# Kernel optimization log

Measured on AMD Instinct MI355X. Metric: run time of the kernel, lower is better.

Reference implementation:

```python
import jax, jax.numpy as jnp
import numpy as np

D = 1024      # input_dim == attention_dim == num_heads*head_dim
H = 16        # num_heads
HD = 64       # head_dim
FF = 4096     # ff_dim
EPS = 1e-5


def _layernorm(x, gamma, beta):
    mu = jnp.mean(x, axis=-1, keepdims=True)
    var = jnp.var(x, axis=-1, keepdims=True)
    return (x - mu) * jax.lax.rsqrt(var + EPS) * gamma + beta


def setup_inputs() -> dict:
    key = jax.random.key(0)
    ks = jax.random.split(key, 11)
    s_in = 1.0 / np.sqrt(D)
    s_ff = 1.0 / np.sqrt(FF)
    return {
        "x": jax.random.normal(ks[0], (2, 2048, D), dtype=jnp.float32),
        "w_qkv": jax.random.uniform(ks[1], (D, 3 * D), jnp.float32, -s_in, s_in),
        "b_qkv": jax.random.uniform(ks[2], (3 * D,), jnp.float32, -s_in, s_in),
        "w_o": jax.random.uniform(ks[3], (D, D), jnp.float32, -s_in, s_in),
        "b_o": jax.random.uniform(ks[4], (D,), jnp.float32, -s_in, s_in),
        "g1": jnp.ones((D,), jnp.float32),
        "be1": jnp.zeros((D,), jnp.float32),
        "w1": jax.random.uniform(ks[5], (D, FF), jnp.float32, -s_in, s_in),
        "b1": jax.random.uniform(ks[6], (FF,), jnp.float32, -s_in, s_in),
        "w2": jax.random.uniform(ks[7], (FF, D), jnp.float32, -s_ff, s_ff),
        "b2": jax.random.uniform(ks[8], (D,), jnp.float32, -s_ff, s_ff),
        "g2": jnp.ones((D,), jnp.float32),
        "be2": jnp.zeros((D,), jnp.float32),
    }


def reference(x, w_qkv, b_qkv, w_o, b_o, g1, be1, w1, b1, w2, b2, g2, be2):
    N, L, _ = x.shape
    qkv = x @ w_qkv + b_qkv                       # [N, L, 3D]
    q = qkv[..., :D].reshape(N, L, H, HD)
    k = qkv[..., D:2 * D].reshape(N, L, H, HD)
    v = qkv[..., 2 * D:].reshape(N, L, H, HD)
    scores = jnp.einsum('nqhd,nkhd->nhqk', q, k) / np.sqrt(HD)
    attn = jax.nn.softmax(scores, axis=-1)        # [N, H, L, L]
    out = jnp.einsum('nhql,nlhd->nqhd', attn, v).reshape(N, L, D)
    attn_out = out @ w_o + b_o
    # dropout is identity in eval mode
    h = _layernorm(attn_out + x, g1, be1)
    ff = jax.nn.relu(h @ w1 + b1) @ w2 + b2
    return _layernorm(h + ff, g2, be2)
```

## Files before the change

### kernel.cpp

```cpp
#include <hip/hip_runtime.h>
#include <cstddef>
#include <cstdint>

static constexpr int Dm   = 1024;
static constexpr int Hh   = 16;
static constexpr int HDd  = 64;
static constexpr int FFd  = 4096;
static constexpr int Ls   = 2048;
static constexpr int Nb   = 2;
static constexpr int Mrows = Nb * Ls;

typedef short bf16x8 __attribute__((ext_vector_type(8)));
typedef float f32x4  __attribute__((ext_vector_type(4)));

__device__ __forceinline__ ushort f2b(float f) {
    uint32_t u = __builtin_bit_cast(uint32_t, f);
    u = (u + 0x7FFFu + ((u >> 16) & 1u)) >> 16;
    return (ushort)u;
}
__device__ __forceinline__ ushort f2bf(float f) {
    return (ushort)((__builtin_bit_cast(uint32_t, f) + 0x8000u) >> 16);
}
__device__ __forceinline__ float b2f(ushort b) {
    return __builtin_bit_cast(float, (uint32_t)b << 16);
}

__device__ __forceinline__ void gl2lds16(const ushort* g, ushort* l) {
    __builtin_amdgcn_global_load_lds(
        (const __attribute__((address_space(1))) void*)g,
        (__attribute__((address_space(3))) void*)l, 16, 0, 0);
}

__global__ __launch_bounds__(256) void convert_bf16(
    const float* __restrict__ src, ushort* __restrict__ dst, int n)
{
    int i = (blockIdx.x * 256 + threadIdx.x) * 4;
    if (i >= n) return;
    float4 v = *(const float4*)(src + i);
    uint2 o;
    o.x = (uint32_t)f2b(v.x) | ((uint32_t)f2b(v.y) << 16);
    o.y = (uint32_t)f2b(v.z) | ((uint32_t)f2b(v.w) << 16);
    *(uint2*)(dst + i) = o;
}

__global__ __launch_bounds__(256) void transpose_bf16(
    const float* __restrict__ src, ushort* __restrict__ dst, int K, int N)
{
    __shared__ float t[32][33];
    const int k0 = blockIdx.y * 32, n0 = blockIdx.x * 32;
    const int tx = threadIdx.x & 31, ty = threadIdx.x >> 5;
    #pragma unroll
    for (int i = 0; i < 4; ++i)
        t[ty + i * 8][tx] = src[(size_t)(k0 + ty + i * 8) * N + n0 + tx];
    __syncthreads();
    #pragma unroll
    for (int i = 0; i < 4; ++i)
        dst[(size_t)(n0 + ty + i * 8) * K + k0 + tx] = f2b(t[tx][ty + i * 8]);
}

template <int TN, int RELU, int VOUT>
__global__ __launch_bounds__(256) void gemm_mfma(
    const ushort* __restrict__ A, const ushort* __restrict__ Bt,
    const float* __restrict__ bias,
    ushort* __restrict__ Cb, ushort* __restrict__ vT, int M, int N, int K)
{
    constexpr int NT  = TN / 32;
    constexpr int BSZ = TN * 32;
    __shared__ __align__(16) ushort As[2 * 128 * 32];
    __shared__ __align__(16) ushort Bs[2 * BSZ];

    const int tid  = threadIdx.x;
    const int bm   = blockIdx.y * 128, bn = blockIdx.x * TN;
    const int wave = tid >> 6, lane = tid & 63;
    const int wm = (wave & 1) * 64;
    const int wn = (wave >> 1) * (TN / 2);
    const int lr = lane & 15, lq = lane >> 4;

    const int rr = wave * 16 + (lane >> 2);
    const int sg = lane & 3;
    const ushort* Ag = A  + (size_t)(bm + rr) * K + sg * 8;
    const ushort* Bg = Bt + (size_t)(bn + rr) * K + sg * 8;

    f32x4 acc[4][NT];
    #pragma unroll
    for (int i = 0; i < 4; ++i)
        #pragma unroll
        for (int j = 0; j < NT; ++j)
            acc[i][j] = (f32x4){0.f, 0.f, 0.f, 0.f};

    gl2lds16(Ag,                  As + wave * 512);
    gl2lds16(Ag + (size_t)64 * K, As + 2048 + wave * 512);
    gl2lds16(Bg,                  Bs + wave * 512);
    if (TN == 128)
        gl2lds16(Bg + (size_t)64 * K, Bs + 2048 + wave * 512);

    int ib = 0;
    for (int k0 = 0; k0 < K; k0 += 32, ib ^= 1) {
        __syncthreads();
        if (k0 + 32 < K) {
            const int nb = ib ^ 1;
            gl2lds16(Ag + k0 + 32,                  As + nb * 4096 + wave * 512);
            gl2lds16(Ag + k0 + 32 + (size_t)64 * K, As + nb * 4096 + 2048 + wave * 512);
            gl2lds16(Bg + k0 + 32,                  Bs + nb * BSZ + wave * 512);
            if (TN == 128)
                gl2lds16(Bg + k0 + 32 + (size_t)64 * K, Bs + nb * BSZ + 2048 + wave * 512);
        }

        const ushort* Ar = As + ib * 4096;
        const ushort* Br = Bs + ib * BSZ;
        bf16x8 af[4], bf[NT];
        #pragma unroll
        for (int mt = 0; mt < 4; ++mt)
            af[mt] = *(const bf16x8*)(Ar + (wm + mt * 16 + lr) * 32 + lq * 8);
        #pragma unroll
        for (int nt = 0; nt < NT; ++nt)
            bf[nt] = *(const bf16x8*)(Br + (wn + nt * 16 + lr) * 32 + lq * 8);

        #pragma unroll
        for (int mt = 0; mt < 4; ++mt)
            #pragma unroll
            for (int nt = 0; nt < NT; ++nt)
                acc[mt][nt] = __builtin_amdgcn_mfma_f32_16x16x32_bf16(
                    af[mt], bf[nt], acc[mt][nt], 0, 0, 0);
    }

    if (VOUT && bn >= 2 * Dm) {
        #pragma unroll
        for (int nt = 0; nt < NT; ++nt) {
            const int n = bn + wn + nt * 16 + lr;
            const float bv = bias[n];
            const int col = n - 2 * Dm;
            const int h = col >> 6, d = col & 63;
            #pragma unroll
            for (int mt = 0; mt < 4; ++mt) {
                const int m0 = bm + wm + mt * 16 + lq * 4;
                const int batch = m0 >> 11, key0 = m0 & (Ls - 1);
                ushort4 ob;
                ushort* op = (ushort*)&ob;
                #pragma unroll
                for (int r = 0; r < 4; ++r) op[r] = f2bf(acc[mt][nt][r] + bv);
                *(ushort4*)(vT + (((size_t)(batch * Hh + h)) * HDd + d) * Ls + key0) = ob;
            }
        }
        return;
    }
    #pragma unroll
    for (int nt = 0; nt < NT; ++nt) {
        const int n = bn + wn + nt * 16 + lr;
        const float bv = bias[n];
        #pragma unroll
        for (int mt = 0; mt < 4; ++mt) {
            const int m0 = bm + wm + mt * 16 + lq * 4;
            #pragma unroll
            for (int r = 0; r < 4; ++r) {
                float v = acc[mt][nt][r] + bv;
                if (RELU) v = fmaxf(v, 0.0f);
                Cb[(size_t)(m0 + r) * N + n] = f2bf(v);
            }
        }
    }
}

__global__ __launch_bounds__(256) void attn_mfma(
    const ushort* __restrict__ qkv, const ushort* __restrict__ vT,
    ushort* __restrict__ out)
{
    const int tid = threadIdx.x, wave = tid >> 6, lane = tid & 63;
    const int lr = lane & 15, lq = lane >> 4;
    const int h = blockIdx.y, n = blockIdx.z;
    const int q0 = blockIdx.x * 128 + wave * 32;
    const size_t RS = 3 * Dm;
    const ushort* base  = qkv + (size_t)n * Ls * RS;
    const ushort* vbase = vT + (size_t)(n * Hh + h) * HDd * Ls;

    __shared__ __align__(16) ushort Kb[64 * 72];
    __shared__ __align__(16) ushort Vt[64 * 72];
    __shared__ __align__(16) ushort Pq[4][32 * 72];

    bf16x8 qf[2][2];
    {
        const float c = 0.18033688011112042f;
        #pragma unroll
        for (int qh = 0; qh < 2; ++qh) {
            const ushort* qg = base + (size_t)(q0 + qh * 16 + lr) * RS + h * HDd + lq * 8;
            bf16x8 t0 = *(const bf16x8*)(qg);
            bf16x8 t1 = *(const bf16x8*)(qg + 32);
            #pragma unroll
            for (int j = 0; j < 8; ++j) {
                qf[0][qh][j] = (short)f2b(b2f((ushort)t0[j]) * c);
                qf[1][qh][j] = (short)f2b(b2f((ushort)t1[j]) * c);
            }
        }
    }

    bf16x8 onesf;
    #pragma unroll
    for (int j = 0; j < 8; ++j) onesf[j] = (short)0x3F80;
    const f32x4 z4 = (f32x4){0.f, 0.f, 0.f, 0.f};

    f32x4 o[4][2];
    #pragma unroll
    for (int dt = 0; dt < 4; ++dt)
        #pragma unroll
        for (int qh = 0; qh < 2; ++qh)
            o[dt][qh] = (f32x4){0.f, 0.f, 0.f, 0.f};
    f32x4 dacc[2];
    dacc[0] = (f32x4){0.f, 0.f, 0.f, 0.f};
    dacc[1] = (f32x4){0.f, 0.f, 0.f, 0.f};

    const int srow = tid >> 2, ssg = tid & 3;
    const ushort* kg = base + (size_t)srow * RS + Dm + h * HDd;
    const ushort* vg = vbase + (size_t)srow * Ls;
    ushort* Pw = Pq[wave];

    int4 ka = *(const int4*)(kg + ssg * 8);
    int4 kb = *(const int4*)(kg + (ssg + 4) * 8);
    int4 va = *(const int4*)(vg + ssg * 8);
    int4 vb = *(const int4*)(vg + (ssg + 4) * 8);

    for (int kt = 0; kt < Ls; kt += 64) {
        __syncthreads();
        *(int4*)(Kb + srow * 72 + ssg * 8)       = ka;
        *(int4*)(Kb + srow * 72 + (ssg + 4) * 8) = kb;
        *(int4*)(Vt + srow * 72 + ssg * 8)       = va;
        *(int4*)(Vt + srow * 72 + (ssg + 4) * 8) = vb;
        __syncthreads();

        if (kt + 64 < Ls) {
            const ushort* kp = kg + (size_t)(kt + 64) * RS;
            const ushort* vp = vg + (kt + 64);
            ka = *(const int4*)(kp + ssg * 8);
            kb = *(const int4*)(kp + (ssg + 4) * 8);
            va = *(const int4*)(vp + ssg * 8);
            vb = *(const int4*)(vp + (ssg + 4) * 8);
        }

        f32x4 s[4][2];
        #pragma unroll
        for (int ks = 0; ks < 2; ++ks)
            #pragma unroll
            for (int mt = 0; mt < 4; ++mt) {
                bf16x8 kf = *(const bf16x8*)(Kb + (mt * 16 + lr) * 72 + ks * 32 + lq * 8);
                #pragma unroll
                for (int qh = 0; qh < 2; ++qh)
                    s[mt][qh] = __builtin_amdgcn_mfma_f32_16x16x32_bf16(
                        kf, qf[ks][qh], ks == 0 ? z4 : s[mt][qh], 0, 0, 0);
            }

        uint2 pb[4][2];
        #pragma unroll
        for (int mt = 0; mt < 4; ++mt)
            #pragma unroll
            for (int qh = 0; qh < 2; ++qh) {
                float p0 = exp2f(s[mt][qh][0]);
                float p1 = exp2f(s[mt][qh][1]);
                float p2 = exp2f(s[mt][qh][2]);
                float p3 = exp2f(s[mt][qh][3]);
                uint32_t w0, w1;
                asm("v_cvt_pk_bf16_f32 %0, %1, %2" : "=v"(w0) : "v"(p0), "v"(p1));
                asm("v_cvt_pk_bf16_f32 %0, %1, %2" : "=v"(w1) : "v"(p2), "v"(p3));
                pb[mt][qh].x = w0;
                pb[mt][qh].y = w1;
            }

        #pragma unroll
        for (int qh = 0; qh < 2; ++qh)
            #pragma unroll
            for (int mt = 0; mt < 4; ++mt)
                *(uint2*)(Pw + (qh * 16 + lr) * 72 + mt * 16 + lq * 4) = pb[mt][qh];

        #pragma unroll
        for (int ks = 0; ks < 2; ++ks) {
            bf16x8 pf[2];
            #pragma unroll
            for (int qh = 0; qh < 2; ++qh)
                pf[qh] = *(const bf16x8*)(Pw + (qh * 16 + lr) * 72 + ks * 32 + lq * 8);
            #pragma unroll
            for (int dt = 0; dt < 4; ++dt) {
                bf16x8 vf = *(const bf16x8*)(Vt + (dt * 16 + lr) * 72 + ks * 32 + lq * 8);
                #pragma unroll
                for (int qh = 0; qh < 2; ++qh)
                    o[dt][qh] = __builtin_amdgcn_mfma_f32_16x16x32_bf16(
                        vf, pf[qh], o[dt][qh], 0, 0, 0);
            }
            #pragma unroll
            for (int qh = 0; qh < 2; ++qh)
                dacc[qh] = __builtin_amdgcn_mfma_f32_16x16x32_bf16(
                    onesf, pf[qh], dacc[qh], 0, 0, 0);
        }
    }

    #pragma unroll
    for (int qh = 0; qh < 2; ++qh) {
        const float inv = 1.0f / dacc[qh][0];
        ushort* orow = out + (size_t)(n * Ls + q0 + qh * 16 + lr) * Dm + h * HDd;
        #pragma unroll
        for (int dt = 0; dt < 4; ++dt) {
            ushort4 ob;
            ushort* op = (ushort*)&ob;
            #pragma unroll
            for (int r = 0; r < 4; ++r) op[r] = f2bf(o[dt][qh][r] * inv);
            *(ushort4*)(orow + dt * 16 + lq * 4) = ob;
        }
    }
}

template <int A_BF16, int B_BF16, int OUT_F32>
__global__ __launch_bounds__(256) void add_ln(
    const void* __restrict__ a, const void* __restrict__ b,
    const float* __restrict__ gamma, const float* __restrict__ beta,
    float* __restrict__ outf, ushort* __restrict__ outb)
{
    const int row = blockIdx.x;
    const int tid = threadIdx.x;

    float va[4], vb[4];
    if (A_BF16) {
        ushort4 u = ((const ushort4*)((const ushort*)a + (size_t)row * Dm))[tid];
        va[0] = b2f(u.x); va[1] = b2f(u.y); va[2] = b2f(u.z); va[3] = b2f(u.w);
    } else {
        float4 f = ((const float4*)((const float*)a + (size_t)row * Dm))[tid];
        va[0] = f.x; va[1] = f.y; va[2] = f.z; va[3] = f.w;
    }
    if (B_BF16) {
        ushort4 u = ((const ushort4*)((const ushort*)b + (size_t)row * Dm))[tid];
        vb[0] = b2f(u.x); vb[1] = b2f(u.y); vb[2] = b2f(u.z); vb[3] = b2f(u.w);
    } else {
        float4 f = ((const float4*)((const float*)b + (size_t)row * Dm))[tid];
        vb[0] = f.x; vb[1] = f.y; vb[2] = f.z; vb[3] = f.w;
    }
    float v[4] = {va[0] + vb[0], va[1] + vb[1], va[2] + vb[2], va[3] + vb[3]};

    float s  = v[0] + v[1] + v[2] + v[3];
    float sq = v[0]*v[0] + v[1]*v[1] + v[2]*v[2] + v[3]*v[3];

    __shared__ float red[8];
    #pragma unroll
    for (int off = 32; off > 0; off >>= 1) {
        s  += __shfl_down(s, off);
        sq += __shfl_down(sq, off);
    }
    const int wv = tid >> 6;
    if ((tid & 63) == 0) { red[wv] = s; red[4 + wv] = sq; }
    __syncthreads();
    s  = red[0] + red[1] + red[2] + red[3];
    sq = red[4] + red[5] + red[6] + red[7];

    const float mu  = s * (1.0f / Dm);
    const float var = sq * (1.0f / Dm) - mu * mu;
    const float inv = rsqrtf(var + 1e-5f);

    const float4 g  = ((const float4*)gamma)[tid];
    const float4 be = ((const float4*)beta)[tid];
    float ov[4];
    ov[0] = (v[0] - mu) * inv * g.x + be.x;
    ov[1] = (v[1] - mu) * inv * g.y + be.y;
    ov[2] = (v[2] - mu) * inv * g.z + be.z;
    ov[3] = (v[3] - mu) * inv * g.w + be.w;
    if (OUT_F32) {
        float4 o4 = {ov[0], ov[1], ov[2], ov[3]};
        ((float4*)(outf + (size_t)row * Dm))[tid] = o4;
    } else {
        uint2 ob;
        ob.x = (uint32_t)f2bf(ov[0]) | ((uint32_t)f2bf(ov[1]) << 16);
        ob.y = (uint32_t)f2bf(ov[2]) | ((uint32_t)f2bf(ov[3]) << 16);
        *(uint2*)(outb + (size_t)row * Dm + tid * 4) = ob;
    }
}

extern "C" void kernel_launch(void* const* d_in, const int* in_sizes, int n_in,
                              void* d_out, int out_size, void* d_ws, size_t ws_size,
                              hipStream_t stream)
{
    const float* x     = (const float*)d_in[0];
    const float* w_qkv = (const float*)d_in[1];
    const float* b_qkv = (const float*)d_in[2];
    const float* w_o   = (const float*)d_in[3];
    const float* b_o   = (const float*)d_in[4];
    const float* g1    = (const float*)d_in[5];
    const float* be1   = (const float*)d_in[6];
    const float* w1    = (const float*)d_in[7];
    const float* b1    = (const float*)d_in[8];
    const float* w2    = (const float*)d_in[9];
    const float* b2    = (const float*)d_in[10];
    const float* g2    = (const float*)d_in[11];
    const float* be2   = (const float*)d_in[12];
    float* out = (float*)d_out;

    char* p = (char*)d_ws;
    ushort* qkvb  = (ushort*)p;  p += (size_t)Mrows * 3 * Dm * 2;
    ushort* attnb = (ushort*)p;  p += (size_t)Mrows * Dm * 2;
    ushort* projb = (ushort*)p;  p += (size_t)Mrows * Dm * 2;
    ushort* hb    = (ushort*)p;  p += (size_t)Mrows * Dm * 2;
    ushort* ffb   = (ushort*)p;  p += (size_t)Mrows * FFd * 2;
    ushort* ff2b  = (ushort*)p;  p += (size_t)Mrows * Dm * 2;
    ushort* xb    = (ushort*)p;  p += (size_t)Mrows * Dm * 2;
    ushort* wqkvT = (ushort*)p;  p += (size_t)(3 * Dm) * Dm * 2;
    ushort* woT   = (ushort*)p;  p += (size_t)Dm * Dm * 2;
    ushort* w1T   = (ushort*)p;  p += (size_t)FFd * Dm * 2;
    ushort* w2T   = (ushort*)p;  p += (size_t)Dm * FFd * 2;
    ushort* vTg   = (ushort*)p;  p += (size_t)Mrows * Dm * 2;

    convert_bf16<<<dim3(Mrows * Dm / 1024), dim3(256), 0, stream>>>(x, xb, Mrows * Dm);
    transpose_bf16<<<dim3(3 * Dm / 32, Dm / 32), dim3(256), 0, stream>>>(w_qkv, wqkvT, Dm, 3 * Dm);
    transpose_bf16<<<dim3(Dm / 32, Dm / 32),     dim3(256), 0, stream>>>(w_o, woT, Dm, Dm);
    transpose_bf16<<<dim3(FFd / 32, Dm / 32),    dim3(256), 0, stream>>>(w1, w1T, Dm, FFd);
    transpose_bf16<<<dim3(Dm / 32, FFd / 32),    dim3(256), 0, stream>>>(w2, w2T, FFd, Dm);

    gemm_mfma<128, 0, 1><<<dim3(3 * Dm / 128, Mrows / 128), dim3(256), 0, stream>>>(
        xb, wqkvT, b_qkv, qkvb, vTg, Mrows, 3 * Dm, Dm);

    attn_mfma<<<dim3(Ls / 128, Hh, Nb), dim3(256), 0, stream>>>(qkvb, vTg, attnb);

    gemm_mfma<64, 0, 0><<<dim3(Dm / 64, Mrows / 128), dim3(256), 0, stream>>>(
        attnb, woT, b_o, projb, nullptr, Mrows, Dm, Dm);

    add_ln<1, 0, 0><<<dim3(Mrows), dim3(256), 0, stream>>>(projb, x, g1, be1, nullptr, hb);

    gemm_mfma<128, 1, 0><<<dim3(FFd / 128, Mrows / 128), dim3(256), 0, stream>>>(
        hb, w1T, b1, ffb, nullptr, Mrows, FFd, Dm);

    gemm_mfma<64, 0, 0><<<dim3(Dm / 64, Mrows / 128), dim3(256), 0, stream>>>(
        ffb, w2T, b2, ff2b, nullptr, Mrows, Dm, FFd);

    add_ln<1, 1, 1><<<dim3(Mrows), dim3(256), 0, stream>>>(ff2b, hb, g2, be2, out, nullptr);
}
```

Before: 402.4 us.

## Split-K the N=1024 GEMMs, fold partial sums and bias into LayerNorm, swizzle blocks

```diff
diff --git a/kernel.cpp b/kernel.cpp
--- a/kernel.cpp
+++ b/kernel.cpp
@@ -58,7 +58,7 @@
         dst[(size_t)(n0 + ty + i * 8) * K + k0 + tx] = f2b(t[tx][ty + i * 8]);
 }
 
-template <int TN, int RELU, int VOUT>
+template <int TN, int RELU, int VOUT, int SPLITK>
 __global__ __launch_bounds__(256) void gemm_mfma(
     const ushort* __restrict__ A, const ushort* __restrict__ Bt,
     const float* __restrict__ bias,
@@ -70,16 +70,27 @@
     __shared__ __align__(16) ushort Bs[2 * BSZ];
 
     const int tid  = threadIdx.x;
-    const int bm   = blockIdx.y * 128, bn = blockIdx.x * TN;
+    int bx, by;
+    {
+        const int gx = gridDim.x;
+        const int nwg = gx * gridDim.y;
+        const int lin = blockIdx.y * gx + blockIdx.x;
+        const int swz = (lin & 7) * (nwg >> 3) + (lin >> 3);
+        by = swz / gx; bx = swz - by * gx;
+    }
+    const int bm   = by * 128, bn = bx * TN;
     const int wave = tid >> 6, lane = tid & 63;
     const int wm = (wave & 1) * 64;
     const int wn = (wave >> 1) * (TN / 2);
     const int lr = lane & 15, lq = lane >> 4;
 
+    const int KS   = K / SPLITK;
+    const int Koff = (SPLITK > 1) ? blockIdx.z * KS : 0;
+
     const int rr = wave * 16 + (lane >> 2);
     const int sg = lane & 3;
-    const ushort* Ag = A  + (size_t)(bm + rr) * K + sg * 8;
-    const ushort* Bg = Bt + (size_t)(bn + rr) * K + sg * 8;
+    const ushort* Ag = A  + (size_t)(bm + rr) * K + Koff + sg * 8;
+    const ushort* Bg = Bt + (size_t)(bn + rr) * K + Koff + sg * 8;
 
     f32x4 acc[4][NT];
     #pragma unroll
@@ -95,9 +106,9 @@
         gl2lds16(Bg + (size_t)64 * K, Bs + 2048 + wave * 512);
 
     int ib = 0;
-    for (int k0 = 0; k0 < K; k0 += 32, ib ^= 1) {
+    for (int k0 = 0; k0 < KS; k0 += 32, ib ^= 1) {
         __syncthreads();
-        if (k0 + 32 < K) {
+        if (k0 + 32 < KS) {
             const int nb = ib ^ 1;
             gl2lds16(Ag + k0 + 32,                  As + nb * 4096 + wave * 512);
             gl2lds16(Ag + k0 + 32 + (size_t)64 * K, As + nb * 4096 + 2048 + wave * 512);
@@ -124,6 +135,21 @@
                     af[mt], bf[nt], acc[mt][nt], 0, 0, 0);
     }
 
+    if (SPLITK > 1) {
+        ushort* Cp = Cb + (size_t)blockIdx.z * M * N;
+        #pragma unroll
+        for (int nt = 0; nt < NT; ++nt) {
+            const int n = bn + wn + nt * 16 + lr;
+            #pragma unroll
+            for (int mt = 0; mt < 4; ++mt) {
+                const int m0 = bm + wm + mt * 16 + lq * 4;
+                #pragma unroll
+                for (int r = 0; r < 4; ++r)
+                    Cp[(size_t)(m0 + r) * N + n] = f2bf(acc[mt][nt][r]);
+            }
+        }
+        return;
+    }
     if (VOUT && bn >= 2 * Dm) {
         #pragma unroll
         for (int nt = 0; nt < NT; ++nt) {
@@ -167,8 +193,13 @@
 {
     const int tid = threadIdx.x, wave = tid >> 6, lane = tid & 63;
     const int lr = lane & 15, lq = lane >> 4;
-    const int h = blockIdx.y, n = blockIdx.z;
-    const int q0 = blockIdx.x * 128 + wave * 32;
+    int bx, h, n;
+    {
+        const int lin = (blockIdx.z * 16 + blockIdx.y) * 16 + blockIdx.x;
+        const int swz = (lin & 7) * 64 + (lin >> 3);
+        bx = swz & 15; h = (swz >> 4) & 15; n = swz >> 8;
+    }
+    const int q0 = bx * 128 + wave * 32;
     const size_t RS = 3 * Dm;
     const ushort* base  = qkv + (size_t)n * Ls * RS;
     const ushort* vbase = vT + (size_t)(n * Hh + h) * HDd * Ls;
@@ -305,31 +336,33 @@
     }
 }
 
-template <int A_BF16, int B_BF16, int OUT_F32>
-__global__ __launch_bounds__(256) void add_ln(
-    const void* __restrict__ a, const void* __restrict__ b,
+template <int OTHER_BF16, int OUT_F32>
+__global__ __launch_bounds__(256) void add3_ln(
+    const ushort* __restrict__ part, const void* __restrict__ other,
+    const float* __restrict__ bias,
     const float* __restrict__ gamma, const float* __restrict__ beta,
     float* __restrict__ outf, ushort* __restrict__ outb)
 {
     const int row = blockIdx.x;
     const int tid = threadIdx.x;
 
-    float va[4], vb[4];
-    if (A_BF16) {
-        ushort4 u = ((const ushort4*)((const ushort*)a + (size_t)row * Dm))[tid];
-        va[0] = b2f(u.x); va[1] = b2f(u.y); va[2] = b2f(u.z); va[3] = b2f(u.w);
+    ushort4 u0 = ((const ushort4*)(part + (size_t)row * Dm))[tid];
+    ushort4 u1 = ((const ushort4*)(part + (size_t)Mrows * Dm + (size_t)row * Dm))[tid];
+    float4  bv = ((const float4*)bias)[tid];
+
+    float vo[4];
+    if (OTHER_BF16) {
+        ushort4 u = ((const ushort4*)((const ushort*)other + (size_t)row * Dm))[tid];
+        vo[0] = b2f(u.x); vo[1] = b2f(u.y); vo[2] = b2f(u.z); vo[3] = b2f(u.w);
     } else {
-        float4 f = ((const float4*)((const float*)a + (size_t)row * Dm))[tid];
-        va[0] = f.x; va[1] = f.y; va[2] = f.z; va[3] = f.w;
-    }
-    if (B_BF16) {
-        ushort4 u = ((const ushort4*)((const ushort*)b + (size_t)row * Dm))[tid];
-        vb[0] = b2f(u.x); vb[1] = b2f(u.y); vb[2] = b2f(u.z); vb[3] = b2f(u.w);
-    } else {
-        float4 f = ((const float4*)((const float*)b + (size_t)row * Dm))[tid];
-        vb[0] = f.x; vb[1] = f.y; vb[2] = f.z; vb[3] = f.w;
-    }
-    float v[4] = {va[0] + vb[0], va[1] + vb[1], va[2] + vb[2], va[3] + vb[3]};
+        float4 f = ((const float4*)((const float*)other + (size_t)row * Dm))[tid];
+        vo[0] = f.x; vo[1] = f.y; vo[2] = f.z; vo[3] = f.w;
+    }
+    float v[4];
+    v[0] = b2f(u0.x) + b2f(u1.x) + bv.x + vo[0];
+    v[1] = b2f(u0.y) + b2f(u1.y) + bv.y + vo[1];
+    v[2] = b2f(u0.z) + b2f(u1.z) + bv.z + vo[2];
+    v[3] = b2f(u0.w) + b2f(u1.w) + bv.w + vo[3];
 
     float s  = v[0] + v[1] + v[2] + v[3];
     float sq = v[0]*v[0] + v[1]*v[1] + v[2]*v[2] + v[3]*v[3];
@@ -390,10 +423,9 @@
     char* p = (char*)d_ws;
     ushort* qkvb  = (ushort*)p;  p += (size_t)Mrows * 3 * Dm * 2;
     ushort* attnb = (ushort*)p;  p += (size_t)Mrows * Dm * 2;
-    ushort* projb = (ushort*)p;  p += (size_t)Mrows * Dm * 2;
+    ushort* part  = (ushort*)p;  p += (size_t)2 * Mrows * Dm * 2;
     ushort* hb    = (ushort*)p;  p += (size_t)Mrows * Dm * 2;
     ushort* ffb   = (ushort*)p;  p += (size_t)Mrows * FFd * 2;
-    ushort* ff2b  = (ushort*)p;  p += (size_t)Mrows * Dm * 2;
     ushort* xb    = (ushort*)p;  p += (size_t)Mrows * Dm * 2;
     ushort* wqkvT = (ushort*)p;  p += (size_t)(3 * Dm) * Dm * 2;
     ushort* woT   = (ushort*)p;  p += (size_t)Dm * Dm * 2;
@@ -407,21 +439,23 @@
     transpose_bf16<<<dim3(FFd / 32, Dm / 32),    dim3(256), 0, stream>>>(w1, w1T, Dm, FFd);
     transpose_bf16<<<dim3(Dm / 32, FFd / 32),    dim3(256), 0, stream>>>(w2, w2T, FFd, Dm);
 
-    gemm_mfma<128, 0, 1><<<dim3(3 * Dm / 128, Mrows / 128), dim3(256), 0, stream>>>(
+    gemm_mfma<128, 0, 1, 1><<<dim3(3 * Dm / 128, Mrows / 128), dim3(256), 0, stream>>>(
         xb, wqkvT, b_qkv, qkvb, vTg, Mrows, 3 * Dm, Dm);
 
     attn_mfma<<<dim3(Ls / 128, Hh, Nb), dim3(256), 0, stream>>>(qkvb, vTg, attnb);
 
-    gemm_mfma<64, 0, 0><<<dim3(Dm / 64, Mrows / 128), dim3(256), 0, stream>>>(
-        attnb, woT, b_o, projb, nullptr, Mrows, Dm, Dm);
-
-    add_ln<1, 0, 0><<<dim3(Mrows), dim3(256), 0, stream>>>(projb, x, g1, be1, nullptr, hb);
-
-    gemm_mfma<128, 1, 0><<<dim3(FFd / 128, Mrows / 128), dim3(256), 0, stream>>>(
+    gemm_mfma<64, 0, 0, 2><<<dim3(Dm / 64, Mrows / 128, 2), dim3(256), 0, stream>>>(
+        attnb, woT, nullptr, part, nullptr, Mrows, Dm, Dm);
+
+    add3_ln<0, 0><<<dim3(Mrows), dim3(256), 0, stream>>>(
+        part, x, b_o, g1, be1, nullptr, hb);
+
+    gemm_mfma<128, 1, 0, 1><<<dim3(FFd / 128, Mrows / 128), dim3(256), 0, stream>>>(
         hb, w1T, b1, ffb, nullptr, Mrows, FFd, Dm);
 
-    gemm_mfma<64, 0, 0><<<dim3(Dm / 64, Mrows / 128), dim3(256), 0, stream>>>(
-        ffb, w2T, b2, ff2b, nullptr, Mrows, Dm, FFd);
-
-    add_ln<1, 1, 1><<<dim3(Mrows), dim3(256), 0, stream>>>(ff2b, hb, g2, be2, out, nullptr);
-}
+    gemm_mfma<64, 0, 0, 2><<<dim3(Dm / 64, Mrows / 128, 2), dim3(256), 0, stream>>>(
+        ffb, w2T, nullptr, part, nullptr, Mrows, Dm, FFd);
+
+    add3_ln<1, 1><<<dim3(Mrows), dim3(256), 0, stream>>>(
+        part, hb, b2, g2, be2, out, nullptr);
+}
```

After: 386.0 us. -4.1%, faster.
